# Kernel optimization log

Hardware: AMD Instinct MI355X
Metric: run time of the kernel (lower is better)

The kernel has to match this reference:

```python
import jax, jax.numpy as jnp
import numpy as np

NUM_HEADS = 16

def setup_inputs() -> dict:
    key = jax.random.key(0)
    ks = jax.random.split(key, 9)
    B, S, H = 2, 2048, 1024
    sc = 0.02
    return {
        "x":  jax.random.normal(ks[0], (B, S, H), jnp.float32),
        "Wq": jax.random.normal(ks[1], (H, H), jnp.float32) * sc,
        "bq": jnp.zeros((H,), jnp.float32),
        "Wk": jax.random.normal(ks[2], (H, H), jnp.float32) * sc,
        "bk": jnp.zeros((H,), jnp.float32),
        "Wv": jax.random.normal(ks[3], (H, H), jnp.float32) * sc,
        "bv": jnp.zeros((H,), jnp.float32),
        "Wo": jax.random.normal(ks[4], (H, H), jnp.float32) * sc,
        "bo": jnp.zeros((H,), jnp.float32),
    }

def _split_heads(t, nh):
    B, S, H = t.shape
    return t.reshape(B, S, nh, H // nh).transpose(0, 2, 1, 3)  # [B, nh, S, hd]

def reference(x, Wq, bq, Wk, bk, Wv, bv, Wo, bo):
    # mask_type == 'gaussian', dropout = 0 (eval), return_weights = False
    B, S, H = x.shape
    nh = NUM_HEADS
    q = _split_heads(x @ Wq + bq, nh)  # [B, nh, S, hd]
    k = _split_heads(x @ Wk + bk, nh)
    v = _split_heads(x @ Wv + bv, nh)
    dif = q - k  # elementwise, as in the original
    # exp(-dif @ dif^T / 2)
    score = jnp.exp(-0.5 * jnp.einsum('bhqd,bhkd->bhqk', dif, dif))
    # gaussian mask: 1 strictly above the diagonal, 0 on/below (faithful to source)
    mask = jnp.triu(jnp.ones((S, S), x.dtype), k=1)
    prob = score * mask  # [B, nh, S, S]
    ctx = jnp.einsum('bhqk,bhkd->bhqd', prob, v)  # [B, nh, S, hd]
    ctx = ctx.transpose(0, 2, 1, 3).reshape(B, S, H)
    return ctx @ Wo + bo
```

## Files before the change

kernel.cpp:

```cpp
#include <hip/hip_runtime.h>
#include <math.h>

constexpr int SEQ  = 2048;
constexpr int HID  = 1024;
constexpr int MTOT = 4096;
constexpr int BH   = 32;

typedef _Float16 f16;
typedef _Float16 f16x4 __attribute__((ext_vector_type(4)));
typedef _Float16 f16x8 __attribute__((ext_vector_type(8)));
typedef float    f32x4 __attribute__((ext_vector_type(4)));

__device__ __forceinline__ void gld16(const f16* g, f16* l) {
    __builtin_amdgcn_global_load_lds(
        (__attribute__((address_space(1))) void*)g,
        (__attribute__((address_space(3))) void*)l, 16, 0, 0);
}

__global__ __launch_bounds__(256) void prep(const float* __restrict__ x,
                                            const float* __restrict__ Wq,
                                            const float* __restrict__ Wk,
                                            const float* __restrict__ Wv,
                                            const float* __restrict__ Wo,
                                            f16* __restrict__ xh,
                                            f16* __restrict__ WqkT,
                                            f16* __restrict__ WvT,
                                            f16* __restrict__ WoT) {
    __shared__ f16 T[64][72];
    const int z = blockIdx.z;
    const int t = threadIdx.x;

    if (z == 3) {
        const int chunk = blockIdx.y * 16 + blockIdx.x;
        const float* src = x + (size_t)chunk * 16384;
        f16* dst = xh + (size_t)chunk * 16384;
#pragma unroll
        for (int it = 0; it < 16; it++) {
            const int i = it * 1024 + t * 4;
            float4 v = *(const float4*)(src + i);
            f16 o[4] = {(f16)v.x, (f16)v.y, (f16)v.z, (f16)v.w};
            *(ushort4*)(dst + i) = *(ushort4*)o;
        }
        return;
    }

    const float* W  = (z == 0) ? Wq : (z == 1) ? Wv : Wo;
    f16* WT = (z == 0) ? WqkT : (z == 1) ? WvT : WoT;
    const int k0 = blockIdx.x * 64, n0 = blockIdx.y * 64;
    const int r  = t >> 4;
    const int c4 = (t & 15) * 4;
#pragma unroll
    for (int rr = 0; rr < 64; rr += 16) {
        float4 w = *(const float4*)(W + (size_t)(k0 + rr + r) * HID + n0 + c4);
        if (z == 0) {
            float4 w2 = *(const float4*)(Wk + (size_t)(k0 + rr + r) * HID + n0 + c4);
            w.x -= w2.x; w.y -= w2.y; w.z -= w2.z; w.w -= w2.w;
        }
        T[c4 + 0][rr + r] = (f16)w.x;
        T[c4 + 1][rr + r] = (f16)w.y;
        T[c4 + 2][rr + r] = (f16)w.z;
        T[c4 + 3][rr + r] = (f16)w.w;
    }
    __syncthreads();
#pragma unroll
    for (int pp = 0; pp < 2; pp++) {
        const int nr = pp * 32 + (t >> 3);
        const int kc = (t & 7) * 8;
        *(uint4*)(WT + (size_t)(n0 + nr) * HID + k0 + kc) = *(uint4*)(&T[nr][kc]);
    }
}

__global__ __launch_bounds__(256, 4) void proj_gemm(const f16* __restrict__ A,
                                                    const f16* __restrict__ WqkT,
                                                    const f16* __restrict__ WvT,
                                                    const float* __restrict__ bq,
                                                    const float* __restrict__ bk,
                                                    const float* __restrict__ bv,
                                                    f16* __restrict__ dif,
                                                    f16* __restrict__ vT) {
    __shared__ f16 As[128 * 72];
    __shared__ f16 Bs[64 * 64];
    const int t = threadIdx.x;
    const int m0  = blockIdx.x * 128;
    const int n0g = blockIdx.y * 64;
    const bool isv = (n0g >= HID);
    const f16* BT = isv ? WvT : WqkT;
    const int n0 = n0g & (HID - 1);
    const int w = t >> 6, l = t & 63, quad = l >> 4, ln = l & 15;
    const int wm = w * 32;
    const int xk = ln & 7;

    const int srow8 = l >> 3;
    const int soct  = (l & 7) ^ srow8;
    const f16* pa = A  + (size_t)(m0 + w * 32 + srow8) * HID + soct * 8;
    const f16* pb = BT + (size_t)(n0 + w * 16 + srow8) * HID + soct * 8;

    f32x4 acc[2][4] = {};

    for (int k0 = 0; k0 < HID; k0 += 64) {
        __syncthreads();
#pragma unroll
        for (int c = 0; c < 4; c++)
            gld16(pa + (size_t)c * 8 * HID + k0, As + (w * 4 + c) * 512);
#pragma unroll
        for (int c = 0; c < 2; c++)
            gld16(pb + (size_t)c * 8 * HID + k0, Bs + (w * 2 + c) * 512);
        __syncthreads();

#pragma unroll
        for (int kh = 0; kh < 2; kh++) {
            f16x8 af[2], bf[4];
#pragma unroll
            for (int mt = 0; mt < 2; mt++) {
                const int row = wm + mt * 16 + ln;
                const int oct = (kh * 4 + quad) ^ xk;
                af[mt] = *(const f16x8*)(As + row * 64 + oct * 8);
            }
#pragma unroll
            for (int nt = 0; nt < 4; nt++) {
                const int row = nt * 16 + ln;
                const int oct = (kh * 4 + quad) ^ xk;
                bf[nt] = *(const f16x8*)(Bs + row * 64 + oct * 8);
            }
#pragma unroll
            for (int mt = 0; mt < 2; mt++)
#pragma unroll
                for (int nt = 0; nt < 4; nt++)
                    acc[mt][nt] = __builtin_amdgcn_mfma_f32_16x16x32_f16(
                        af[mt], bf[nt], acc[mt][nt], 0, 0, 0);
        }
    }

    __syncthreads();
    const int b_  = m0 >> 11;
    const int s0g = m0 & 2047;
    const int h_  = n0 >> 6;

    if (!isv) {
        float bb[4];
#pragma unroll
        for (int nt = 0; nt < 4; nt++) {
            const int nl = n0 + nt * 16 + ln;
            bb[nt] = bq[nl] - bk[nl];
        }
#pragma unroll
        for (int mt = 0; mt < 2; mt++)
#pragma unroll
            for (int nt = 0; nt < 4; nt++)
#pragma unroll
                for (int r = 0; r < 4; r++) {
                    const int sl = wm + mt * 16 + quad * 4 + r;
                    As[sl * 72 + nt * 16 + ln] = (f16)(acc[mt][nt][r] + bb[nt]);
                }
        __syncthreads();
        f16* base = dif + ((size_t)(b_ * 16 + h_) * SEQ + s0g) * 64;
        const int sl = t >> 1, eo = (t & 1) * 32;
#pragma unroll
        for (int i = 0; i < 4; i++)
            *(uint4*)(base + (size_t)sl * 64 + eo + i * 8) =
                *(uint4*)(&As[sl * 72 + eo + i * 8]);
    } else {
        float bb[4];
#pragma unroll
        for (int nt = 0; nt < 4; nt++)
            bb[nt] = bv[n0 + nt * 16 + ln];
#pragma unroll
        for (int mt = 0; mt < 2; mt++)
#pragma unroll
            for (int nt = 0; nt < 4; nt++)
#pragma unroll
                for (int r = 0; r < 4; r++) {
                    const int sl = wm + mt * 16 + quad * 4 + r;
                    As[(nt * 16 + ln) * 136 + sl] = (f16)(acc[mt][nt][r] + bb[nt]);
                }
        __syncthreads();
        const int eb = t >> 2, so = (t & 3) * 32;
        f16* base = vT + ((size_t)(b_ * 16 + h_) * 64 + eb) * SEQ + s0g + so;
#pragma unroll
        for (int i = 0; i < 4; i++)
            *(uint4*)(base + i * 8) = *(uint4*)(&As[eb * 136 + so + i * 8]);
    }
}

__global__ __launch_bounds__(256) void out_gemm(const f16* __restrict__ C0,
                                                const f16* __restrict__ C1,
                                                const f16* __restrict__ WoT,
                                                const float* __restrict__ bo,
                                                float* __restrict__ out) {
    __shared__ f16 As[2][128 * 72];
    __shared__ f16 Bs[2][64 * 72];
    const int t = threadIdx.x;
    const int m0 = blockIdx.x * 128, n0 = blockIdx.y * 64;
    const int w = t >> 6, l = t & 63, quad = l >> 4, ln = l & 15;
    const int wm = (w >> 1) * 64, wn = (w & 1) * 32;
    const int arow = t >> 1, ahalf = (t & 1) * 32;
    const int brow = t >> 2, boff = (t & 3) * 16;

    const f16* pa0 = C0  + (size_t)(m0 + arow) * HID + ahalf;
    const f16* pa1 = C1  + (size_t)(m0 + arow) * HID + ahalf;
    const f16* pb  = WoT + (size_t)(n0 + brow) * HID + boff;

    f16x8 a0 = *(const f16x8*)(pa0)      + *(const f16x8*)(pa1);
    f16x8 a1 = *(const f16x8*)(pa0 + 8)  + *(const f16x8*)(pa1 + 8);
    f16x8 a2 = *(const f16x8*)(pa0 + 16) + *(const f16x8*)(pa1 + 16);
    f16x8 a3 = *(const f16x8*)(pa0 + 24) + *(const f16x8*)(pa1 + 24);
    uint4 b0 = *(const uint4*)(pb), b1 = *(const uint4*)(pb + 8);

    f32x4 acc[4][2] = {};
    int buf = 0;

    for (int k0 = 0; k0 < HID; k0 += 64) {
        f16* da = As[buf] + arow * 72 + ahalf;
        *(f16x8*)(da)      = a0; *(f16x8*)(da + 8)  = a1;
        *(f16x8*)(da + 16) = a2; *(f16x8*)(da + 24) = a3;
        f16* db = Bs[buf] + brow * 72 + boff;
        *(uint4*)(db) = b0; *(uint4*)(db + 8) = b1;
        __syncthreads();
        if (k0 + 64 < HID) {
            const int kn = k0 + 64;
            a0 = *(const f16x8*)(pa0 + kn)      + *(const f16x8*)(pa1 + kn);
            a1 = *(const f16x8*)(pa0 + kn + 8)  + *(const f16x8*)(pa1 + kn + 8);
            a2 = *(const f16x8*)(pa0 + kn + 16) + *(const f16x8*)(pa1 + kn + 16);
            a3 = *(const f16x8*)(pa0 + kn + 24) + *(const f16x8*)(pa1 + kn + 24);
            b0 = *(const uint4*)(pb + kn); b1 = *(const uint4*)(pb + kn + 8);
        }
#pragma unroll
        for (int kh = 0; kh < 2; kh++) {
            f16x8 af[4], bf[2];
#pragma unroll
            for (int mt = 0; mt < 4; mt++)
                af[mt] = *(const f16x8*)(As[buf] + (wm + mt * 16 + ln) * 72 + kh * 32 + quad * 8);
#pragma unroll
            for (int nt = 0; nt < 2; nt++)
                bf[nt] = *(const f16x8*)(Bs[buf] + (wn + nt * 16 + ln) * 72 + kh * 32 + quad * 8);
#pragma unroll
            for (int mt = 0; mt < 4; mt++)
#pragma unroll
                for (int nt = 0; nt < 2; nt++)
                    acc[mt][nt] = __builtin_amdgcn_mfma_f32_16x16x32_f16(
                        af[mt], bf[nt], acc[mt][nt], 0, 0, 0);
        }
        buf ^= 1;
    }

#pragma unroll
    for (int mt = 0; mt < 4; mt++)
#pragma unroll
        for (int nt = 0; nt < 2; nt++) {
            const int n = n0 + wn + nt * 16 + ln;
            const float bb = bo[n];
            const int m_base = m0 + wm + mt * 16 + quad * 4;
#pragma unroll
            for (int r = 0; r < 4; r++)
                out[(size_t)(m_base + r) * HID + n] =
                    acc[mt][nt][r] * 65536.0f + bb;
        }
}

__global__ __launch_bounds__(256, 4) void attn_f16(const f16* __restrict__ dif,
                                                   const f16* __restrict__ vT,
                                                   f16* __restrict__ ctx0,
                                                   f16* __restrict__ ctx1) {
    __shared__ f16 Qs[64 * 72];
    __shared__ f16 Ks[64 * 72];
    __shared__ f16 Vs[64 * 72];

    const int blk = blockIdx.x;
    const int g   = blk >> 3;
    const int bh  = (blk & 7) * 4 + (g & 3);
    const int pq  = (g >> 2) & 15;
    const int ks  = g >> 6;

    f16* Cout = ks ? ctx1 : ctx0;
    const f16* D  = dif + (size_t)bh * SEQ * 64;
    const f16* VT = vT  + (size_t)bh * 64 * SEQ;
    const int b = bh >> 4, h = bh & 15;
    const int t = threadIdx.x, w = t >> 6, l = t & 63, quad = l >> 4, ln = l & 15;
    const int qh = w >> 1, jh = w & 1;
    const int ve = t >> 2, vc = (t & 3) * 16;

    for (int half = 0; half < 2; half++) {
        const int qt = half ? (31 - pq) : pq;
        const int i0 = qt * 64;
        __syncthreads();

#pragma unroll
        for (int rr = 0; rr < 2; rr++) {
            const int o = rr * 2048 + t * 8;
            uint4 v = *(const uint4*)(D + i0 * 64 + o);
            *(uint4*)(Qs + (o >> 6) * 72 + (o & 63)) = v;
        }
        __syncthreads();
        f16x8 aq[2][2];
#pragma unroll
        for (int mt = 0; mt < 2; mt++)
#pragma unroll
            for (int kh = 0; kh < 2; kh++)
                aq[mt][kh] = *(const f16x8*)(Qs + (qh * 32 + mt * 16 + ln) * 72
                                             + kh * 32 + quad * 8);

        f32x4 acc[2][4] = {};
        const int kt0 = qt + ks;

        uint4 kr0, kr1, vr0, vr1;
        if (kt0 < 32) {
            const int j0 = kt0 * 64;
            kr0 = *(const uint4*)(D + j0 * 64 + t * 8);
            kr1 = *(const uint4*)(D + j0 * 64 + 2048 + t * 8);
            vr0 = *(const uint4*)(VT + (size_t)ve * SEQ + j0 + vc);
            vr1 = *(const uint4*)(VT + (size_t)ve * SEQ + j0 + vc + 8);
        }

        for (int kt = kt0; kt < 32; kt += 2) {
            const int j0 = kt * 64;
            __syncthreads();

            {
                const int o0 = t * 8, o1 = 2048 + t * 8;
                *(uint4*)(Ks + (o0 >> 6) * 72 + (o0 & 63)) = kr0;
                *(uint4*)(Ks + (o1 >> 6) * 72 + (o1 & 63)) = kr1;
                *(uint4*)(Vs + ve * 72 + vc)     = vr0;
                *(uint4*)(Vs + ve * 72 + vc + 8) = vr1;
            }
            __syncthreads();

            if (kt + 2 < 32) {
                const int j2 = (kt + 2) * 64;
                kr0 = *(const uint4*)(D + j2 * 64 + t * 8);
                kr1 = *(const uint4*)(D + j2 * 64 + 2048 + t * 8);
                vr0 = *(const uint4*)(VT + (size_t)ve * SEQ + j2 + vc);
                vr1 = *(const uint4*)(VT + (size_t)ve * SEQ + j2 + vc + 8);
            }

            f32x4 st[2][2] = {};
#pragma unroll
            for (int kh = 0; kh < 2; kh++)
#pragma unroll
                for (int nt = 0; nt < 2; nt++) {
                    f16x8 ak = *(const f16x8*)(Ks + (jh * 32 + nt * 16 + ln) * 72
                                               + kh * 32 + quad * 8);
#pragma unroll
                    for (int mt = 0; mt < 2; mt++)
                        st[nt][mt] = __builtin_amdgcn_mfma_f32_16x16x32_f16(
                            ak, aq[mt][kh], st[nt][mt], 0, 0, 0);
                }

            const bool full = (kt > qt);
            f16x4 pf[2][2];
#pragma unroll
            for (int nt = 0; nt < 2; nt++)
#pragma unroll
                for (int mt = 0; mt < 2; mt++) {
                    const int gi = i0 + qh * 32 + mt * 16 + ln;
#pragma unroll
                    for (int r = 0; r < 4; r++) {
                        const int gj = j0 + jh * 32 + nt * 16 + quad * 4 + r;
                        float p = (full || (gj > gi))
                                      ? fminf(__expf(fmaf(st[nt][mt][r], -0.5f,
                                                          -11.090354888959125f)),
                                              60000.0f)
                                      : 0.0f;
                        pf[nt][mt][r] = (f16)p;
                    }
                }

#pragma unroll
            for (int nt = 0; nt < 2; nt++)
#pragma unroll
                for (int nte = 0; nte < 4; nte++) {
                    f16x4 bv = *(const f16x4*)(Vs + (nte * 16 + ln) * 72
                                               + jh * 32 + nt * 16 + quad * 4);
#pragma unroll
                    for (int mt = 0; mt < 2; mt++)
                        acc[mt][nte] = __builtin_amdgcn_mfma_f32_16x16x16f16(
                            pf[nt][mt], bv, acc[mt][nte], 0, 0, 0);
                }
        }

        __syncthreads();
        if (jh == 1) {
#pragma unroll
            for (int mt = 0; mt < 2; mt++)
#pragma unroll
                for (int nte = 0; nte < 4; nte++)
#pragma unroll
                    for (int r = 0; r < 4; r++)
                        Qs[(qh * 32 + mt * 16 + quad * 4 + r) * 72 + nte * 16 + ln] =
                            (f16)acc[mt][nte][r];
        }
        __syncthreads();
        if (jh == 0) {
#pragma unroll
            for (int mt = 0; mt < 2; mt++)
#pragma unroll
                for (int nte = 0; nte < 4; nte++)
#pragma unroll
                    for (int r = 0; r < 4; r++) {
                        const int iloc = qh * 32 + mt * 16 + quad * 4 + r;
                        float v = acc[mt][nte][r]
                                + (float)Qs[iloc * 72 + nte * 16 + ln];
                        Cout[(size_t)(b * SEQ + i0 + iloc) * HID + h * 64
                             + nte * 16 + ln] = (f16)v;
                    }
        }
    }
}

extern "C" void kernel_launch(void* const* d_in, const int* in_sizes, int n_in,
                              void* d_out, int out_size, void* d_ws, size_t ws_size,
                              hipStream_t stream) {
    const float* x  = (const float*)d_in[0];
    const float* Wq = (const float*)d_in[1];
    const float* bq = (const float*)d_in[2];
    const float* Wk = (const float*)d_in[3];
    const float* bk = (const float*)d_in[4];
    const float* Wv = (const float*)d_in[5];
    const float* bv = (const float*)d_in[6];
    const float* Wo = (const float*)d_in[7];
    const float* bo = (const float*)d_in[8];
    float* out = (float*)d_out;

    char* ws = (char*)d_ws;
    f16* xh   = (f16*)(ws);
    f16* WqkT = (f16*)(ws + (8 << 20));
    f16* WvT  = (f16*)(ws + (10 << 20));
    f16* WoT  = (f16*)(ws + (12 << 20));
    f16* dif  = (f16*)(ws + (14 << 20));
    f16* vT   = (f16*)(ws + (22 << 20));
    f16* ctx0 = (f16*)(ws + (30 << 20));
    f16* ctx1 = (f16*)(ws + (38 << 20));

    prep<<<dim3(16, 16, 4), 256, 0, stream>>>(x, Wq, Wk, Wv, Wo,
                                              xh, WqkT, WvT, WoT);
    proj_gemm<<<dim3(MTOT / 128, 32), 256, 0, stream>>>(xh, WqkT, WvT,
                                                        bq, bk, bv, dif, vT);
    attn_f16<<<1024, 256, 0, stream>>>(dif, vT, ctx0, ctx1);
    out_gemm<<<dim3(MTOT / 128, 16), 256, 0, stream>>>(ctx0, ctx1, WoT, bo, out);
}
```

Before: 185.8 us.

## Use direct global-to-LDS loads with double-buffered XOR-swizzled K/V tiles

The attention kernel now loads Q, K and V tiles straight into shared memory with global_load_lds, replacing the register-staged copies. K and V go into two alternating buffers, so each tile of the next iteration is fetched while the current one is being computed, which removes one barrier per iteration. Padded 72-wide rows are replaced by 64-wide rows with an XOR swizzle to avoid LDS bank conflicts. Shared memory grows from about 27 KB to about 40 KB per block, which may reduce the number of resident blocks per CU. Correctness also depends on the global_load_lds transfers having completed by the time each barrier is reached.

```diff
diff --git a/kernel.cpp b/kernel.cpp
--- a/kernel.cpp
+++ b/kernel.cpp
@@ -261,9 +261,8 @@
                                                    const f16* __restrict__ vT,
                                                    f16* __restrict__ ctx0,
                                                    f16* __restrict__ ctx1) {
-    __shared__ f16 Qs[64 * 72];
-    __shared__ f16 Ks[64 * 72];
-    __shared__ f16 Vs[64 * 72];
+    __shared__ f16 Qs[64 * 64];
+    __shared__ f16 KV[2][2 * 64 * 64];
 
     const int blk = blockIdx.x;
     const int g   = blk >> 3;
@@ -277,7 +276,10 @@
     const int b = bh >> 4, h = bh & 15;
     const int t = threadIdx.x, w = t >> 6, l = t & 63, quad = l >> 4, ln = l & 15;
     const int qh = w >> 1, jh = w & 1;
-    const int ve = t >> 2, vc = (t & 3) * 16;
+    const int xk = ln & 7;
+
+    const int srow = l >> 3;
+    const int soct = (l & 7) ^ srow;
 
     for (int half = 0; half < 2; half++) {
         const int qt = half ? (31 - pq) : pq;
@@ -285,60 +287,59 @@
         __syncthreads();
 
 #pragma unroll
-        for (int rr = 0; rr < 2; rr++) {
-            const int o = rr * 2048 + t * 8;
-            uint4 v = *(const uint4*)(D + i0 * 64 + o);
-            *(uint4*)(Qs + (o >> 6) * 72 + (o & 63)) = v;
-        }
-        __syncthreads();
+        for (int c = 0; c < 2; c++)
+            gld16(D + (size_t)(i0 + w * 16 + c * 8 + srow) * 64 + soct * 8,
+                  Qs + (w * 16 + c * 8) * 64);
+        const int kt0 = qt + ks;
+        const int nit = (kt0 < 32) ? (32 - kt0 + 1) / 2 : 0;
+        if (nit > 0) {
+            const int j0 = kt0 * 64;
+#pragma unroll
+            for (int c = 0; c < 2; c++) {
+                gld16(D + (size_t)(j0 + w * 16 + c * 8 + srow) * 64 + soct * 8,
+                      KV[0] + (w * 16 + c * 8) * 64);
+                gld16(VT + (size_t)(w * 16 + c * 8 + srow) * SEQ + j0 + soct * 8,
+                      KV[0] + 4096 + (w * 16 + c * 8) * 64);
+            }
+        }
+        __syncthreads();
+
         f16x8 aq[2][2];
 #pragma unroll
         for (int mt = 0; mt < 2; mt++)
 #pragma unroll
             for (int kh = 0; kh < 2; kh++)
-                aq[mt][kh] = *(const f16x8*)(Qs + (qh * 32 + mt * 16 + ln) * 72
-                                             + kh * 32 + quad * 8);
+                aq[mt][kh] = *(const f16x8*)(Qs + (qh * 32 + mt * 16 + ln) * 64
+                                             + ((kh * 4 + quad) ^ xk) * 8);
 
         f32x4 acc[2][4] = {};
-        const int kt0 = qt + ks;
-
-        uint4 kr0, kr1, vr0, vr1;
-        if (kt0 < 32) {
-            const int j0 = kt0 * 64;
-            kr0 = *(const uint4*)(D + j0 * 64 + t * 8);
-            kr1 = *(const uint4*)(D + j0 * 64 + 2048 + t * 8);
-            vr0 = *(const uint4*)(VT + (size_t)ve * SEQ + j0 + vc);
-            vr1 = *(const uint4*)(VT + (size_t)ve * SEQ + j0 + vc + 8);
-        }
-
-        for (int kt = kt0; kt < 32; kt += 2) {
+
+        for (int it = 0; it < nit; it++) {
+            const int kt = kt0 + it * 2;
             const int j0 = kt * 64;
-            __syncthreads();
-
-            {
-                const int o0 = t * 8, o1 = 2048 + t * 8;
-                *(uint4*)(Ks + (o0 >> 6) * 72 + (o0 & 63)) = kr0;
-                *(uint4*)(Ks + (o1 >> 6) * 72 + (o1 & 63)) = kr1;
-                *(uint4*)(Vs + ve * 72 + vc)     = vr0;
-                *(uint4*)(Vs + ve * 72 + vc + 8) = vr1;
+            const f16* Ks = KV[it & 1];
+            const f16* Vs = KV[it & 1] + 4096;
+
+            if (it + 1 < nit) {
+                const int j2 = j0 + 128;
+                f16* Kn = KV[(it + 1) & 1];
+#pragma unroll
+                for (int c = 0; c < 2; c++) {
+                    gld16(D + (size_t)(j2 + w * 16 + c * 8 + srow) * 64 + soct * 8,
+                          Kn + (w * 16 + c * 8) * 64);
+                    gld16(VT + (size_t)(w * 16 + c * 8 + srow) * SEQ + j2 + soct * 8,
+                          Kn + 4096 + (w * 16 + c * 8) * 64);
+                }
             }
-            __syncthreads();
-
-            if (kt + 2 < 32) {
-                const int j2 = (kt + 2) * 64;
-                kr0 = *(const uint4*)(D + j2 * 64 + t * 8);
-                kr1 = *(const uint4*)(D + j2 * 64 + 2048 + t * 8);
-                vr0 = *(const uint4*)(VT + (size_t)ve * SEQ + j2 + vc);
-                vr1 = *(const uint4*)(VT + (size_t)ve * SEQ + j2 + vc + 8);
-            }
 
             f32x4 st[2][2] = {};
 #pragma unroll
             for (int kh = 0; kh < 2; kh++)
 #pragma unroll
                 for (int nt = 0; nt < 2; nt++) {
-                    f16x8 ak = *(const f16x8*)(Ks + (jh * 32 + nt * 16 + ln) * 72
-                                               + kh * 32 + quad * 8);
+                    const int row = jh * 32 + nt * 16 + ln;
+                    f16x8 ak = *(const f16x8*)(Ks + row * 64
+                                               + ((kh * 4 + quad) ^ xk) * 8);
 #pragma unroll
                     for (int mt = 0; mt < 2; mt++)
                         st[nt][mt] = __builtin_amdgcn_mfma_f32_16x16x32_f16(
@@ -368,25 +369,31 @@
             for (int nt = 0; nt < 2; nt++)
 #pragma unroll
                 for (int nte = 0; nte < 4; nte++) {
-                    f16x4 bv = *(const f16x4*)(Vs + (nte * 16 + ln) * 72
-                                               + jh * 32 + nt * 16 + quad * 4);
+                    const int row = nte * 16 + ln;
+                    const int octl = jh * 4 + nt * 2 + (quad >> 1);
+                    f16x4 bv = *(const f16x4*)(Vs + row * 64
+                                               + (octl ^ xk) * 8 + (quad & 1) * 4);
 #pragma unroll
                     for (int mt = 0; mt < 2; mt++)
                         acc[mt][nte] = __builtin_amdgcn_mfma_f32_16x16x16f16(
                             pf[nt][mt], bv, acc[mt][nte], 0, 0, 0);
                 }
-        }
-
-        __syncthreads();
+
+            __syncthreads();
+        }
+
         if (jh == 1) {
 #pragma unroll
             for (int mt = 0; mt < 2; mt++)
 #pragma unroll
                 for (int nte = 0; nte < 4; nte++)
 #pragma unroll
-                    for (int r = 0; r < 4; r++)
-                        Qs[(qh * 32 + mt * 16 + quad * 4 + r) * 72 + nte * 16 + ln] =
+                    for (int r = 0; r < 4; r++) {
+                        const int row = qh * 32 + mt * 16 + quad * 4 + r;
+                        const int c   = nte * 16 + ln;
+                        Qs[row * 64 + (((c >> 3) ^ (row & 7)) * 8) + (c & 7)] =
                             (f16)acc[mt][nte][r];
+                    }
         }
         __syncthreads();
         if (jh == 0) {
@@ -396,11 +403,11 @@
                 for (int nte = 0; nte < 4; nte++)
 #pragma unroll
                     for (int r = 0; r < 4; r++) {
-                        const int iloc = qh * 32 + mt * 16 + quad * 4 + r;
+                        const int row = qh * 32 + mt * 16 + quad * 4 + r;
+                        const int c   = nte * 16 + ln;
                         float v = acc[mt][nte][r]
-                                + (float)Qs[iloc * 72 + nte * 16 + ln];
-                        Cout[(size_t)(b * SEQ + i0 + iloc) * HID + h * 64
-                             + nte * 16 + ln] = (f16)v;
+                                + (float)Qs[row * 64 + (((c >> 3) ^ (row & 7)) * 8) + (c & 7)];
+                        Cout[(size_t)(b * SEQ + i0 + row) * HID + h * 64 + c] = (f16)v;
                     }
         }
     }
```

New measurement: 196.4 us. 5.8% more time.
